# Optimization experiments

Measured on AMD Instinct MI355X. Metric: run time of the kernel, lower is better.

## Reference

```python
import jax, jax.numpy as jnp
import numpy as np

N, K, D = 65536, 1024, 512


def setup_inputs() -> dict:
    key = jax.random.key(0)
    kx, kc, kv, kp = jax.random.split(key, 4)
    X = jax.random.normal(kx, (N, D), dtype=jnp.float32)
    center = jax.random.normal(kc, (K, D), dtype=jnp.float32)
    var = jax.random.uniform(kv, (K,), dtype=jnp.float32)
    pr = jax.random.uniform(kp, (K,), dtype=jnp.float32)
    threshold = jnp.zeros((1,), dtype=jnp.float32)
    return {"X": X, "center": center, "var": var, "pr": pr, "threshold": threshold}


def reference(X, center, var, pr, threshold):
    # Pairwise squared distances [N, K] via the expanded form
    # avoids materializing the N x K x D tensor).
    x_sq = jnp.sum(X * X, axis=-1, keepdims=True)            # [N, 1]
    c_sq = jnp.sum(center * center, axis=-1)                  # [K]
    cross = jnp.einsum('nd,kd->nk', X, center)                # [N, K]
    sqdist = x_sq - 2.0 * cross + c_sq[None, :]               # [N, K]
    # density: reciprocal-distance weighted sum with weights pr * var
    density = jnp.reciprocal(sqdist) @ (pr * var)             # [N]
    return density - threshold                                 # [N] (threshold [1] broadcasts)
```

## Files before the change

kernel.cpp:

```cpp
#include <hip/hip_runtime.h>
#include <stdint.h>


#define NR 65536
#define KC 1024
#define DD 512

#define BM 256
#define BN 256
#define BK 64
#define NKT (DD / BK)
#define NPART (KC / BN)

#define SLOT_SZ 65536
#define PART_OFF 131072
#define LDS_TOTAL (PART_OFF + 4096)

typedef __bf16 bf16;
typedef __attribute__((ext_vector_type(4))) __bf16 bf16x4;
typedef __attribute__((ext_vector_type(8))) __bf16 bf16x8;
typedef __attribute__((ext_vector_type(4))) float f32x4;

__device__ __forceinline__ void gload16(const void* g, void* l) {
  __builtin_amdgcn_global_load_lds(
      (const __attribute__((address_space(1))) unsigned int*)g,
      (__attribute__((address_space(3))) unsigned int*)l, 16, 0, 0);
}

__global__ __launch_bounds__(256) void prep_kernel(
    const float* __restrict__ X, const float* __restrict__ C,
    const float* __restrict__ var, const float* __restrict__ pr,
    bf16* __restrict__ Xb, bf16* __restrict__ Cb,
    float* __restrict__ xsq, float* __restrict__ csq, float* __restrict__ w) {
  const int row  = (int)((blockIdx.x * 256 + threadIdx.x) >> 6);
  const int lane = (int)(threadIdx.x & 63);
  const bool isX = row < NR;
  const float* srow = isX ? (X + (size_t)row * DD) : (C + (size_t)(row - NR) * DD);
  bf16* drow = isX ? (Xb + (size_t)row * DD) : (Cb + (size_t)(row - NR) * DD);

  float4 a = reinterpret_cast<const float4*>(srow)[lane];
  float4 b = reinterpret_cast<const float4*>(srow)[64 + lane];
  float s = a.x * a.x + a.y * a.y + a.z * a.z + a.w * a.w +
            b.x * b.x + b.y * b.y + b.z * b.z + b.w * b.w;
#pragma unroll
  for (int off = 1; off < 64; off <<= 1) s += __shfl_xor(s, off, 64);

  bf16x4 va = {(bf16)a.x, (bf16)a.y, (bf16)a.z, (bf16)a.w};
  bf16x4 vb = {(bf16)b.x, (bf16)b.y, (bf16)b.z, (bf16)b.w};
  reinterpret_cast<bf16x4*>(drow)[lane]      = va;
  reinterpret_cast<bf16x4*>(drow)[64 + lane] = vb;

  if (lane == 0) {
    if (isX) {
      xsq[row] = s;
    } else {
      const int k = row - NR;
      csq[k] = s;
      w[k]   = pr[k] * var[k];
    }
  }
}


#define STAGE_A(h, tn, slotW)                                                   \
  gload16(aSrc0 + (size_t)((h) * 64) * DD + (tn) * 64,                          \
          smem + (slotW) + (h) * 16384 + wid * 1024);                           \
  gload16(aSrc0 + (size_t)((h) * 64 + 128) * DD + (tn) * 64,                    \
          smem + (slotW) + (h) * 16384 + 8192 + wid * 1024);

#define STAGE_B(kk, tn, slotW)                                                  \
  gload16(bSrc0 + (tn) * 64 + (kk) * 32,                                        \
          smem + (slotW) + 32768 + (kk) * 16384 + wid * 1024);                  \
  gload16(bSrc0 + (size_t)128 * DD + (tn) * 64 + (kk) * 32,                     \
          smem + (slotW) + 32768 + (kk) * 16384 + 8192 + wid * 1024);

#define READ_B(dst, kk, base)                                                   \
  _Pragma("unroll") for (int n = 0; n < 4; ++n)                                 \
    dst[n] = *(const bf16x8*)(smem + (base) + 32768 + (kk) * 16384 + bRd +      \
                              n * 1024);

__global__ __launch_bounds__(512, 2) void density_kernel(
    const bf16* __restrict__ Xb, const bf16* __restrict__ Cb,
    const float* __restrict__ xsq, const float* __restrict__ csq,
    const float* __restrict__ w, float* __restrict__ partial) {
  extern __shared__ char smem[];

  const int tid  = (int)threadIdx.x;
  const int lane = tid & 63;
  const int wid  = tid >> 6;
  const int wr   = wid >> 2;
  const int wcn  = wid & 3;
  const int lr   = lane & 15;
  const int lc   = lane >> 4;

  const int bid   = (int)blockIdx.x;
  const int swz   = (bid & 7) * 128 + (bid >> 3);
  const int ntile = swz >> 8;
  const int mtile = swz & 255;
  const int rowBase = mtile * BM;
  const int colBase = ntile * BN;

  const bf16* aSrc0 = Xb + (size_t)(rowBase + wid * 8 + (lane >> 3)) * DD +
                      (((lane & 7) ^ (lane >> 3)) << 3);
  const bf16* bSrc0 = Cb + (size_t)(colBase + wid * 16 + (lane >> 2)) * DD +
                      ((((lane & 3) ^ ((lane >> 3) & 3))) << 3);

  const int aRd  = (wr * 64 + lr) * 128;
  const int aSw0 = ((lc ^ (lr & 7)) << 4);
  const int aSw1 = (((4 | lc) ^ (lr & 7)) << 4);
  const int bRd  = (wcn * 64 + lr) * 64 + ((lc ^ ((lr >> 1) & 3)) << 4);

  f32x4 acc[8][4];
#pragma unroll
  for (int m = 0; m < 8; ++m)
#pragma unroll
    for (int n = 0; n < 4; ++n) acc[m][n] = (f32x4){0.f, 0.f, 0.f, 0.f};

  bf16x8 bgK0[4], bgK1[4];

  STAGE_A(0, 0, 0);
  STAGE_B(0, 0, 0);
  STAGE_A(1, 0, 0);
  STAGE_B(1, 0, 0);
  asm volatile("s_waitcnt vmcnt(0)");
  __builtin_amdgcn_s_barrier();

#pragma unroll 1
  for (int t = 0; t < NKT; ++t) {
    const int slotR = (t & 1) << 16;
    const int slotW = slotR ^ SLOT_SZ;
    const int tn = t + 1;
    const bool st = tn < NKT;

    if (st) {
      STAGE_A(0, tn, slotW);
      STAGE_B(0, tn, slotW);
      STAGE_A(1, tn, slotW);
      STAGE_B(1, tn, slotW);
    }

    READ_B(bgK0, 0, slotR);
    READ_B(bgK1, 1, slotR);

    __builtin_amdgcn_s_setprio(1);
#pragma unroll
    for (int h = 0; h < 2; ++h) {
#pragma unroll
      for (int mi = 0; mi < 4; ++mi) {
        const bf16x8 a0 = *(const bf16x8*)(smem + slotR + h * 16384 + aRd +
                                           mi * 2048 + aSw0);
        const bf16x8 a1 = *(const bf16x8*)(smem + slotR + h * 16384 + aRd +
                                           mi * 2048 + aSw1);
#pragma unroll
        for (int n = 0; n < 4; ++n)
          acc[h * 4 + mi][n] = __builtin_amdgcn_mfma_f32_16x16x32_bf16(
              a0, bgK0[n], acc[h * 4 + mi][n], 0, 0, 0);
#pragma unroll
        for (int n = 0; n < 4; ++n)
          acc[h * 4 + mi][n] = __builtin_amdgcn_mfma_f32_16x16x32_bf16(
              a1, bgK1[n], acc[h * 4 + mi][n], 0, 0, 0);
      }
    }
    __builtin_amdgcn_s_setprio(0);

    if (st) {
      asm volatile("s_waitcnt vmcnt(0)");
      __builtin_amdgcn_s_barrier();
    }
  }

  float xr[8][4];
#pragma unroll
  for (int m = 0; m < 8; ++m)
#pragma unroll
    for (int j = 0; j < 4; ++j)
      xr[m][j] = xsq[rowBase + wr * 128 + m * 16 + lc * 4 + j];

  float rsum[8][4];
#pragma unroll
  for (int m = 0; m < 8; ++m)
#pragma unroll
    for (int j = 0; j < 4; ++j) rsum[m][j] = 0.f;

#pragma unroll
  for (int n = 0; n < 4; ++n) {
    const int gc = colBase + wcn * 64 + n * 16 + lr;
    const float cs = csq[gc];
    const float ww = w[gc];
#pragma unroll
    for (int m = 0; m < 8; ++m)
#pragma unroll
      for (int j = 0; j < 4; ++j) {
        const float sq = xr[m][j] + cs - 2.f * acc[m][n][j];
        rsum[m][j] += ww * __builtin_amdgcn_rcpf(sq);
      }
  }
#pragma unroll
  for (int m = 0; m < 8; ++m)
#pragma unroll
    for (int j = 0; j < 4; ++j) {
      float v = rsum[m][j];
      v += __shfl_xor(v, 1, 64);
      v += __shfl_xor(v, 2, 64);
      v += __shfl_xor(v, 4, 64);
      v += __shfl_xor(v, 8, 64);
      rsum[m][j] = v;
    }

  float* part = (float*)(smem + PART_OFF);
  __syncthreads();
  if (lr == 0) {
#pragma unroll
    for (int m = 0; m < 8; ++m)
#pragma unroll
      for (int j = 0; j < 4; ++j)
        part[wcn * 256 + wr * 128 + m * 16 + lc * 4 + j] = rsum[m][j];
  }
  __syncthreads();
  if (tid < BM) {
    const float s = part[tid] + part[256 + tid] + part[512 + tid] + part[768 + tid];
    partial[(size_t)ntile * NR + rowBase + tid] = s;
  }
}

__global__ __launch_bounds__(256) void reduce_kernel(
    const float* __restrict__ partial, const float* __restrict__ thr,
    float* __restrict__ out) {
  const int n = (int)(blockIdx.x * 256 + threadIdx.x);
  float s = 0.f;
#pragma unroll
  for (int g = 0; g < NPART; ++g) s += partial[(size_t)g * NR + n];
  out[n] = s - thr[0];
}

extern "C" void kernel_launch(void* const* d_in, const int* in_sizes, int n_in,
                              void* d_out, int out_size, void* d_ws, size_t ws_size,
                              hipStream_t stream) {
  const float* X   = (const float*)d_in[0];
  const float* C   = (const float*)d_in[1];
  const float* var = (const float*)d_in[2];
  const float* pr  = (const float*)d_in[3];
  const float* thr = (const float*)d_in[4];
  float* out = (float*)d_out;

  char* ws = (char*)d_ws;
  bf16* Xb   = (bf16*)(ws);
  bf16* Cb   = (bf16*)(ws + (size_t)NR * DD * 2);
  float* xsq = (float*)(ws + (size_t)NR * DD * 2 + (size_t)KC * DD * 2);
  float* csq = xsq + NR;
  float* w   = csq + KC;
  float* partial = w + KC;

  prep_kernel<<<(NR + KC) / 4, 256, 0, stream>>>(X, C, var, pr, Xb, Cb, xsq, csq, w);
  density_kernel<<<(NR / BM) * NPART, 512, LDS_TOTAL, stream>>>(
      Xb, Cb, xsq, csq, w, partial);
  reduce_kernel<<<NR / 256, 256, 0, stream>>>(partial, thr, out);
}
```

Baseline: 114.8 us.

## Use 4 waves per block with 128x128 warp tiles in density GEMM

```diff
diff --git a/kernel.cpp b/kernel.cpp
--- a/kernel.cpp
+++ b/kernel.cpp
@@ -14,7 +14,7 @@
 
 #define SLOT_SZ 65536
 #define PART_OFF 131072
-#define LDS_TOTAL (PART_OFF + 4096)
+#define LDS_TOTAL (PART_OFF + 2048)
 
 typedef __bf16 bf16;
 typedef __attribute__((ext_vector_type(4))) __bf16 bf16x4;
@@ -62,24 +62,29 @@
 }
 
 
-#define STAGE_A(h, tn, slotW)                                                   \
-  gload16(aSrc0 + (size_t)((h) * 64) * DD + (tn) * 64,                          \
-          smem + (slotW) + (h) * 16384 + wid * 1024);                           \
-  gload16(aSrc0 + (size_t)((h) * 64 + 128) * DD + (tn) * 64,                    \
-          smem + (slotW) + (h) * 16384 + 8192 + wid * 1024);
-
-#define STAGE_B(kk, tn, slotW)                                                  \
-  gload16(bSrc0 + (tn) * 64 + (kk) * 32,                                        \
-          smem + (slotW) + 32768 + (kk) * 16384 + wid * 1024);                  \
-  gload16(bSrc0 + (size_t)128 * DD + (tn) * 64 + (kk) * 32,                     \
-          smem + (slotW) + 32768 + (kk) * 16384 + 8192 + wid * 1024);
-
-#define READ_B(dst, kk, base)                                                   \
-  _Pragma("unroll") for (int n = 0; n < 4; ++n)                                 \
-    dst[n] = *(const bf16x8*)(smem + (base) + 32768 + (kk) * 16384 + bRd +      \
-                              n * 1024);
-
-__global__ __launch_bounds__(512, 2) void density_kernel(
+#define STAGE_A(h, tn, slotW, w, aS)                                            \
+  gload16(aS + (size_t)((h) * 64) * DD + (tn) * 64,                             \
+          smem + (slotW) + (h) * 16384 + (w) * 1024);                           \
+  gload16(aS + (size_t)((h) * 64 + 128) * DD + (tn) * 64,                       \
+          smem + (slotW) + (h) * 16384 + 8192 + (w) * 1024);
+
+#define STAGE_B(kk, tn, slotW, w, bS)                                           \
+  gload16(bS + (tn) * 64 + (kk) * 32,                                           \
+          smem + (slotW) + 32768 + (kk) * 16384 + (w) * 1024);                  \
+  gload16(bS + (size_t)128 * DD + (tn) * 64 + (kk) * 32,                        \
+          smem + (slotW) + 32768 + (kk) * 16384 + 8192 + (w) * 1024);
+
+#define STAGE_ALL(tn, slotW)                                                    \
+  STAGE_A(0, tn, slotW, wid, aSrcA);                                            \
+  STAGE_A(0, tn, slotW, wid + 4, aSrcB);                                        \
+  STAGE_A(1, tn, slotW, wid, aSrcA);                                            \
+  STAGE_A(1, tn, slotW, wid + 4, aSrcB);                                        \
+  STAGE_B(0, tn, slotW, wid, bSrcA);                                            \
+  STAGE_B(0, tn, slotW, wid + 4, bSrcB);                                        \
+  STAGE_B(1, tn, slotW, wid, bSrcA);                                            \
+  STAGE_B(1, tn, slotW, wid + 4, bSrcB);
+
+__global__ __launch_bounds__(256, 1) void density_kernel(
     const bf16* __restrict__ Xb, const bf16* __restrict__ Cb,
     const float* __restrict__ xsq, const float* __restrict__ csq,
     const float* __restrict__ w, float* __restrict__ partial) {
@@ -88,8 +93,8 @@
   const int tid  = (int)threadIdx.x;
   const int lane = tid & 63;
   const int wid  = tid >> 6;
-  const int wr   = wid >> 2;
-  const int wcn  = wid & 3;
+  const int wr   = wid >> 1;
+  const int wcn  = wid & 1;
   const int lr   = lane & 15;
   const int lc   = lane >> 4;
 
@@ -100,28 +105,25 @@
   const int rowBase = mtile * BM;
   const int colBase = ntile * BN;
 
-  const bf16* aSrc0 = Xb + (size_t)(rowBase + wid * 8 + (lane >> 3)) * DD +
+  const bf16* aSrcA = Xb + (size_t)(rowBase + wid * 8 + (lane >> 3)) * DD +
                       (((lane & 7) ^ (lane >> 3)) << 3);
-  const bf16* bSrc0 = Cb + (size_t)(colBase + wid * 16 + (lane >> 2)) * DD +
+  const bf16* aSrcB = aSrcA + (size_t)32 * DD;
+  const bf16* bSrcA = Cb + (size_t)(colBase + wid * 16 + (lane >> 2)) * DD +
                       ((((lane & 3) ^ ((lane >> 3) & 3))) << 3);
+  const bf16* bSrcB = bSrcA + (size_t)64 * DD;
 
   const int aRd  = (wr * 64 + lr) * 128;
   const int aSw0 = ((lc ^ (lr & 7)) << 4);
   const int aSw1 = (((4 | lc) ^ (lr & 7)) << 4);
-  const int bRd  = (wcn * 64 + lr) * 64 + ((lc ^ ((lr >> 1) & 3)) << 4);
-
-  f32x4 acc[8][4];
-#pragma unroll
-  for (int m = 0; m < 8; ++m)
-#pragma unroll
-    for (int n = 0; n < 4; ++n) acc[m][n] = (f32x4){0.f, 0.f, 0.f, 0.f};
-
-  bf16x8 bgK0[4], bgK1[4];
-
-  STAGE_A(0, 0, 0);
-  STAGE_B(0, 0, 0);
-  STAGE_A(1, 0, 0);
-  STAGE_B(1, 0, 0);
+  const int bRd  = (wcn * 128 + lr) * 64 + ((lc ^ ((lr >> 1) & 3)) << 4);
+
+  f32x4 acc[8][8];
+#pragma unroll
+  for (int m = 0; m < 8; ++m)
+#pragma unroll
+    for (int n = 0; n < 8; ++n) acc[m][n] = (f32x4){0.f, 0.f, 0.f, 0.f};
+
+  STAGE_ALL(0, 0);
   asm volatile("s_waitcnt vmcnt(0)");
   __builtin_amdgcn_s_barrier();
 
@@ -129,18 +131,16 @@
   for (int t = 0; t < NKT; ++t) {
     const int slotR = (t & 1) << 16;
     const int slotW = slotR ^ SLOT_SZ;
-    const int tn = t + 1;
-    const bool st = tn < NKT;
-
-    if (st) {
-      STAGE_A(0, tn, slotW);
-      STAGE_B(0, tn, slotW);
-      STAGE_A(1, tn, slotW);
-      STAGE_B(1, tn, slotW);
-    }
-
-    READ_B(bgK0, 0, slotR);
-    READ_B(bgK1, 1, slotR);
+    const bool st = (t + 1) < NKT;
+
+    if (st) { STAGE_ALL(t + 1, slotW); }
+
+    bf16x8 bgK0[8], bgK1[8];
+#pragma unroll
+    for (int n = 0; n < 8; ++n) {
+      bgK0[n] = *(const bf16x8*)(smem + slotR + 32768 + bRd + n * 1024);
+      bgK1[n] = *(const bf16x8*)(smem + slotR + 32768 + 16384 + bRd + n * 1024);
+    }
 
     __builtin_amdgcn_s_setprio(1);
 #pragma unroll
@@ -152,11 +152,11 @@
         const bf16x8 a1 = *(const bf16x8*)(smem + slotR + h * 16384 + aRd +
                                            mi * 2048 + aSw1);
 #pragma unroll
-        for (int n = 0; n < 4; ++n)
+        for (int n = 0; n < 8; ++n)
           acc[h * 4 + mi][n] = __builtin_amdgcn_mfma_f32_16x16x32_bf16(
               a0, bgK0[n], acc[h * 4 + mi][n], 0, 0, 0);
 #pragma unroll
-        for (int n = 0; n < 4; ++n)
+        for (int n = 0; n < 8; ++n)
           acc[h * 4 + mi][n] = __builtin_amdgcn_mfma_f32_16x16x32_bf16(
               a1, bgK1[n], acc[h * 4 + mi][n], 0, 0, 0);
       }
@@ -169,12 +169,10 @@
     }
   }
 
-  float xr[8][4];
-#pragma unroll
-  for (int m = 0; m < 8; ++m)
-#pragma unroll
-    for (int j = 0; j < 4; ++j)
-      xr[m][j] = xsq[rowBase + wr * 128 + m * 16 + lc * 4 + j];
+  f32x4 xrv[8];
+#pragma unroll
+  for (int m = 0; m < 8; ++m)
+    xrv[m] = *(const f32x4*)(xsq + rowBase + wr * 128 + m * 16 + lc * 4);
 
   float rsum[8][4];
 #pragma unroll
@@ -183,15 +181,15 @@
     for (int j = 0; j < 4; ++j) rsum[m][j] = 0.f;
 
 #pragma unroll
-  for (int n = 0; n < 4; ++n) {
-    const int gc = colBase + wcn * 64 + n * 16 + lr;
+  for (int n = 0; n < 8; ++n) {
+    const int gc = colBase + wcn * 128 + n * 16 + lr;
     const float cs = csq[gc];
     const float ww = w[gc];
 #pragma unroll
     for (int m = 0; m < 8; ++m)
 #pragma unroll
       for (int j = 0; j < 4; ++j) {
-        const float sq = xr[m][j] + cs - 2.f * acc[m][n][j];
+        const float sq = xrv[m][j] + cs - 2.f * acc[m][n][j];
         rsum[m][j] += ww * __builtin_amdgcn_rcpf(sq);
       }
   }
@@ -218,7 +216,7 @@
   }
   __syncthreads();
   if (tid < BM) {
-    const float s = part[tid] + part[256 + tid] + part[512 + tid] + part[768 + tid];
+    const float s = part[tid] + part[256 + tid];
     partial[(size_t)ntile * NR + rowBase + tid] = s;
   }
 }
@@ -252,7 +250,7 @@
   float* partial = w + KC;
 
   prep_kernel<<<(NR + KC) / 4, 256, 0, stream>>>(X, C, var, pr, Xb, Cb, xsq, csq, w);
-  density_kernel<<<(NR / BM) * NPART, 512, LDS_TOTAL, stream>>>(
+  density_kernel<<<(NR / BM) * NPART, 256, LDS_TOTAL, stream>>>(
       Xb, Cb, xsq, csq, w, partial);
   reduce_kernel<<<NR / 256, 256, 0, stream>>>(partial, thr, out);
 }
```

Measured after the change: 160.3 us. +39.7%, slower.
